# Kernel tuning notes

Measured on AMD Instinct MI355X. Metric: run time of the kernel, lower is better.

The kernel has to match this reference:

```python
import jax, jax.numpy as jnp
import numpy as np

N_NODES = 100000


def gcn_conv(x, W, b, src, dst, n_nodes):
    # x: [N, Fin], W: [Fin, Fout], edge (src->dst) with self-loops added,
    # symmetric normalization D^{-1/2} A D^{-1/2} as in PyG GCNConv defaults.
    h = x @ W  # [N, Fout]
    loops = jnp.arange(n_nodes, dtype=src.dtype)
    src_all = jnp.concatenate([src, loops])
    dst_all = jnp.concatenate([dst, loops])
    ones = jnp.ones(src_all.shape[0], dtype=h.dtype)
    deg = jax.ops.segment_sum(ones, dst_all, num_segments=n_nodes)  # in-degree incl. self-loop
    dinv = jnp.where(deg > 0, jax.lax.rsqrt(deg), 0.0)
    norm = dinv[src_all] * dinv[dst_all]  # [E+N]
    msg = h[src_all] * norm[:, None]      # gather + scale
    out = jax.ops.segment_sum(msg, dst_all, num_segments=n_nodes)  # scatter-add
    return out + b


def setup_inputs() -> dict:
    key = jax.random.key(0)
    k1, k2, k3, k4 = jax.random.split(key, 4)
    in_dim, hidden, out_dim = 128, 128, 64
    n_edges = 600000
    x = jax.random.normal(k1, (N_NODES, in_dim), dtype=jnp.float32)
    edge_index = jax.random.randint(k2, (2, n_edges), 0, N_NODES, dtype=jnp.int64)
    # Glorot-ish init for weights
    W1 = jax.random.normal(k3, (in_dim, hidden), dtype=jnp.float32) / np.sqrt(in_dim)
    b1 = jnp.zeros((hidden,), dtype=jnp.float32)
    W2 = jax.random.normal(k4, (hidden, out_dim), dtype=jnp.float32) / np.sqrt(hidden)
    b2 = jnp.zeros((out_dim,), dtype=jnp.float32)
    return {"x": x, "edge_index": edge_index, "W1": W1, "b1": b1, "W2": W2, "b2": b2}


def reference(x, edge_index, W1, b1, W2, b2):
    src, dst = edge_index[0], edge_index[1]
    h = jax.nn.relu(gcn_conv(x, W1, b1, src, dst, N_NODES))
    # dropout is identity in eval mode (training=False)
    return gcn_conv(h, W2, b2, src, dst, N_NODES)
```

## Files before the change

### kernel.cpp

```cpp
#include <hip/hip_runtime.h>
#include <hip/hip_bf16.h>
#include <stdint.h>

typedef unsigned int u32;
typedef unsigned short u16;
typedef __attribute__((ext_vector_type(8))) short short8;
typedef __attribute__((ext_vector_type(4))) float f32x4;

#define SCAN_TILE 2048

__device__ __forceinline__ float bf2f(u16 u) {
    union { u32 u; float f; } v; v.u = ((u32)u) << 16; return v.f;
}
__device__ __forceinline__ u16 f2bf(float f) {
    u32 u = __float_as_uint(f);
    u32 r = (u + 0x7FFFu + ((u >> 16) & 1u)) >> 16;
    return (u16)r;
}
__device__ __forceinline__ u32 packbf(float lo, float hi) {
    return ((u32)f2bf(hi) << 16) | (u32)f2bf(lo);
}

__global__ __launch_bounds__(256) void detect_zero_k(const u32* __restrict__ xw,
                                                     const u32* __restrict__ ew,
                                                     int* __restrict__ flags,
                                                     int* __restrict__ deg, int M) {
    const int t = threadIdx.x;
    const int i4 = (blockIdx.x * 256 + t) * 4;
    if (i4 + 4 <= M) *(int4*)(deg + i4) = make_int4(0, 0, 0, 0);
    else { for (int j = 0; j < 4; j++) if (i4 + j < M) deg[i4 + j] = 0; }

    if (blockIdx.x == 0) {
        __shared__ int cnt;
        __shared__ u32 orr;
        if (t == 0) { cnt = 0; orr = 0u; }
        __syncthreads();
        int hits = 0;
        for (int i = t; i < 1024; i += 256) {
            u32 f = (xw[i] >> 7) & 0xFFu;
            if (f >= 100u && f <= 140u) hits++;
        }
        atomicAdd(&cnt, hits);
        atomicOr(&orr, ew[2 * t + 1]);
        __syncthreads();
        if (t == 0) {
            flags[0] = (cnt < 512) ? 1 : 0;
            flags[1] = (orr == 0u) ? 1 : 0;
        }
    }
}

template<int N>
__device__ __forceinline__ void wpack_one(const void* W, uint4* wpk, int p, int f32w) {
    const int n = p & (N - 1);
    const int kb = p >> ((N == 128) ? 7 : 6);
    u32 pk[4];
    if (f32w) {
        const float* wp = (const float*)W + (size_t)(kb * 8) * N + n;
        #pragma unroll
        for (int jj = 0; jj < 4; jj++)
            pk[jj] = packbf(wp[(2 * jj) * N], wp[(2 * jj + 1) * N]);
    } else {
        const u16* wp = (const u16*)W + (size_t)(kb * 8) * N + n;
        #pragma unroll
        for (int jj = 0; jj < 4; jj++)
            pk[jj] = ((u32)wp[(2 * jj + 1) * N] << 16) | (u32)wp[(2 * jj) * N];
    }
    uint4 v; v.x = pk[0]; v.y = pk[1]; v.z = pk[2]; v.w = pk[3];
    wpk[p] = v;
}

__global__ __launch_bounds__(256) void wpack_all_k(const void* __restrict__ W1,
                                                   const void* __restrict__ W2,
                                                   uint4* __restrict__ wpk1,
                                                   uint4* __restrict__ wpk2,
                                                   const int* __restrict__ flags) {
    const int b = blockIdx.x, t = threadIdx.x;
    const int f32w = flags[0];
    if (b < 8) wpack_one<128>(W1, wpk1, b * 256 + t, f32w);
    else       wpack_one<64> (W2, wpk2, (b - 8) * 256 + t, f32w);
}

__global__ __launch_bounds__(256) void count_deg_k(const void* __restrict__ ei, int E,
                                                   const int* __restrict__ flags,
                                                   int* __restrict__ deg) {
    const int i2 = (blockIdx.x * 256 + threadIdx.x) * 2;
    if (i2 >= E) return;
    if (flags[1]) {
        const long long* dp = (const long long*)ei + E;
        if (i2 + 1 < E) {
            longlong2 v = *(const longlong2*)(dp + i2);
            atomicAdd(&deg[(int)v.x], 1);
            atomicAdd(&deg[(int)v.y], 1);
        } else atomicAdd(&deg[(int)dp[i2]], 1);
    } else {
        const int* dp = (const int*)ei + E;
        if (i2 + 1 < E) {
            int2 v = *(const int2*)(dp + i2);
            atomicAdd(&deg[v.x], 1);
            atomicAdd(&deg[v.y], 1);
        } else atomicAdd(&deg[dp[i2]], 1);
    }
}

__global__ __launch_bounds__(256) void scan_partial_k(const int* __restrict__ deg, int M,
                                                      int* __restrict__ bsum) {
    const int t = threadIdx.x;
    const int base = blockIdx.x * SCAN_TILE + t * 8;
    int s = 0;
    if (base + 8 <= M) {
        int4 a = *(const int4*)(deg + base);
        int4 b = *(const int4*)(deg + base + 4);
        s = a.x + a.y + a.z + a.w + b.x + b.y + b.z + b.w;
    } else {
        for (int j = 0; j < 8; j++) if (base + j < M) s += deg[base + j];
    }
    __shared__ int red[256];
    red[t] = s;
    __syncthreads();
    for (int d = 128; d > 0; d >>= 1) {
        if (t < d) red[t] += red[t + d];
        __syncthreads();
    }
    if (t == 0) bsum[blockIdx.x] = red[0];
}

__global__ __launch_bounds__(256) void scan_bsum_k(int* __restrict__ bsum, int nb,
                                                   int* __restrict__ off, int M) {
    __shared__ int buf[2][256];
    const int t = threadIdx.x;
    int v = (t < nb) ? bsum[t] : 0;
    const int own = v;
    buf[0][t] = v;
    __syncthreads();
    int cur = 0;
    for (int d = 1; d < 256; d <<= 1) {
        int x = buf[cur][t];
        if (t >= d) x += buf[cur][t - d];
        buf[cur ^ 1][t] = x;
        __syncthreads();
        cur ^= 1;
    }
    if (t < nb) bsum[t] = buf[cur][t] - own;
    if (t == 255) off[M] = buf[cur][255];
}

__global__ __launch_bounds__(256) void scan_final_k(const int* __restrict__ deg,
                                                    const int* __restrict__ bsum, int M,
                                                    int* __restrict__ off,
                                                    int* __restrict__ cursor,
                                                    float* __restrict__ dinv) {
    const int t = threadIdx.x;
    const int base = blockIdx.x * SCAN_TILE + t * 8;
    int v[8];
    int s = 0;
    const bool full = (base + 8 <= M);
    if (full) {
        int4 a = *(const int4*)(deg + base);
        int4 b = *(const int4*)(deg + base + 4);
        v[0] = a.x; v[1] = a.y; v[2] = a.z; v[3] = a.w;
        v[4] = b.x; v[5] = b.y; v[6] = b.z; v[7] = b.w;
        s = v[0] + v[1] + v[2] + v[3] + v[4] + v[5] + v[6] + v[7];
    } else {
        #pragma unroll
        for (int j = 0; j < 8; j++) { v[j] = (base + j < M) ? deg[base + j] : 0; s += v[j]; }
    }
    __shared__ int buf[2][256];
    buf[0][t] = s;
    __syncthreads();
    int cur = 0;
    for (int d = 1; d < 256; d <<= 1) {
        int x = buf[cur][t];
        if (t >= d) x += buf[cur][t - d];
        buf[cur ^ 1][t] = x;
        __syncthreads();
        cur ^= 1;
    }
    int pre = bsum[blockIdx.x] + buf[cur][t] - s;
    int o[8]; float dv[8];
    #pragma unroll
    for (int j = 0; j < 8; j++) {
        o[j] = pre;
        dv[j] = rsqrtf((float)(v[j] + 1));
        pre += v[j];
    }
    if (full) {
        *(int4*)(off + base)     = make_int4(o[0], o[1], o[2], o[3]);
        *(int4*)(off + base + 4) = make_int4(o[4], o[5], o[6], o[7]);
        *(int4*)(cursor + base)     = make_int4(o[0], o[1], o[2], o[3]);
        *(int4*)(cursor + base + 4) = make_int4(o[4], o[5], o[6], o[7]);
        *(float4*)(dinv + base)     = make_float4(dv[0], dv[1], dv[2], dv[3]);
        *(float4*)(dinv + base + 4) = make_float4(dv[4], dv[5], dv[6], dv[7]);
    } else {
        for (int j = 0; j < 8; j++) if (base + j < M) {
            off[base + j] = o[j]; cursor[base + j] = o[j]; dinv[base + j] = dv[j];
        }
    }
}

__global__ __launch_bounds__(256) void fill_k(const void* __restrict__ ei, int E,
                                              const int* __restrict__ flags,
                                              int* __restrict__ cursor, int* __restrict__ eidx) {
    const int i2 = (blockIdx.x * 256 + threadIdx.x) * 2;
    if (i2 >= E) return;
    int s0, d0, s1 = -1, d1 = -1;
    if (flags[1]) {
        const long long* sp = (const long long*)ei;
        const long long* dp = sp + E;
        if (i2 + 1 < E) {
            longlong2 sv = *(const longlong2*)(sp + i2);
            longlong2 dv = *(const longlong2*)(dp + i2);
            s0 = (int)sv.x; s1 = (int)sv.y; d0 = (int)dv.x; d1 = (int)dv.y;
        } else { s0 = (int)sp[i2]; d0 = (int)dp[i2]; }
    } else {
        const int* sp = (const int*)ei;
        const int* dp = sp + E;
        if (i2 + 1 < E) {
            int2 sv = *(const int2*)(sp + i2);
            int2 dv = *(const int2*)(dp + i2);
            s0 = sv.x; s1 = sv.y; d0 = dv.x; d1 = dv.y;
        } else { s0 = sp[i2]; d0 = dp[i2]; }
    }
    int p0 = atomicAdd(&cursor[d0], 1);
    eidx[p0] = s0;
    if (s1 >= 0 || d1 >= 0) {
        if (i2 + 1 < E) {
            int p1 = atomicAdd(&cursor[d1], 1);
            eidx[p1] = s1;
        }
    }
}

template<int N>
__global__ __launch_bounds__(256) void gemm_mfma_k(
    const void* __restrict__ X, const uint4* __restrict__ wpk,
    const float* __restrict__ dinv, u16* __restrict__ HS,
    const int* __restrict__ flags, int x_is_ext, int M)
{
    constexpr int NT = N / 16;
    constexpr int NC8 = N / 8;
    __shared__ u32 xlds[64 * 64];
    const int t = threadIdx.x;
    const int wave = t >> 6, lane = t & 63;
    const int q = lane >> 4, m = lane & 15;
    const bool xf32 = (x_is_ext != 0) && (flags[0] != 0);
    const int row0 = blockIdx.x * 64;

    for (int c = t; c < 1024; c += 256) {
        const int row = c >> 4, c8 = c & 15;
        const int grow = row0 + row;
        uint4 pk = make_uint4(0u, 0u, 0u, 0u);
        if (grow < M) {
            if (xf32) {
                const float* xp = (const float*)X + (size_t)grow * 128 + c8 * 8;
                float4 u = *(const float4*)xp;
                float4 v = *(const float4*)(xp + 4);
                pk.x = packbf(u.x, u.y); pk.y = packbf(u.z, u.w);
                pk.z = packbf(v.x, v.y); pk.w = packbf(v.z, v.w);
            } else {
                pk = *(const uint4*)((const u16*)X + (size_t)grow * 128 + c8 * 8);
            }
        }
        *(uint4*)&xlds[row * 64 + c8 * 4] = pk;
    }
    __syncthreads();

    union { uint4 u; short8 v; } a[4];
    #pragma unroll
    for (int s = 0; s < 4; s++)
        a[s].u = *(const uint4*)&xlds[(wave * 16 + m) * 64 + (s * 4 + q) * 4];

    f32x4 acc[NT];
    #pragma unroll
    for (int tt = 0; tt < NT; tt++)
        acc[tt] = (f32x4){0.f, 0.f, 0.f, 0.f};

    #pragma unroll
    for (int s = 0; s < 4; s++) {
        union { uint4 u; short8 v; } b[NT];
        #pragma unroll
        for (int tt = 0; tt < NT; tt++)
            b[tt].u = wpk[(s * 4 + q) * N + tt * 16 + m];
        #pragma unroll
        for (int tt = 0; tt < NT; tt++)
            acc[tt] = __builtin_amdgcn_mfma_f32_16x16x32_bf16(
                a[s].v, b[tt].v, acc[tt], 0, 0, 0);
    }

    float dv[4];
    #pragma unroll
    for (int r = 0; r < 4; r++) {
        const int grow = row0 + wave * 16 + q * 4 + r;
        dv[r] = (grow < M) ? dinv[grow] : 0.f;
    }

    u16* orow = (u16*)&xlds[wave * 16 * 64];
    #pragma unroll
    for (int tt = 0; tt < NT; tt++)
        #pragma unroll
        for (int r = 0; r < 4; r++)
            orow[(q * 4 + r) * N + tt * 16 + m] = f2bf(acc[tt][r] * dv[r]);

    constexpr int ITER = 16 * NC8 / 64;
    #pragma unroll
    for (int j = 0; j < ITER; j++) {
        const int cc = lane + j * 64;
        const int lrow = cc / NC8, c8 = cc % NC8;
        const int grow = row0 + wave * 16 + lrow;
        uint4 v = *(const uint4*)&((const u32*)orow)[lrow * (N / 2) + c8 * 4];
        if (grow < M)
            *(uint4*)(HS + (size_t)grow * N + c8 * 8) = v;
    }
}

template<int N, bool RELU>
__global__ __launch_bounds__(256) void aggregate_k(
    const u16* __restrict__ hs, const int* __restrict__ eidx,
    const int* __restrict__ off, const float* __restrict__ dinv,
    const void* __restrict__ bias, void* __restrict__ out,
    const int* __restrict__ flags, int out_is_ext, int M)
{
    constexpr int TPN = N / 8;
    constexpr int NPB = 256 / TPN;
    const int node = blockIdx.x * NPB + threadIdx.x / TPN;
    const int lane = threadIdx.x % TPN;
    if (node >= M) return;
    const int f32io = flags[0];
    const int beg = off[node], end = off[node + 1];
    const int c8 = lane * 8;
    const u16* __restrict__ hrow = hs + c8;

    float a[8];
    {
        uint4 sp = *(const uint4*)(hrow + (size_t)node * N);
        const u16* s = (const u16*)&sp;
        #pragma unroll
        for (int j = 0; j < 8; j++) a[j] = bf2f(s[j]);
    }

    int p = beg;
    for (; p + 4 <= end; p += 4) {
        const int s0 = eidx[p + 0], s1 = eidx[p + 1];
        const int s2 = eidx[p + 2], s3 = eidx[p + 3];
        uint4 v0 = *(const uint4*)(hrow + (size_t)s0 * N);
        uint4 v1 = *(const uint4*)(hrow + (size_t)s1 * N);
        uint4 v2 = *(const uint4*)(hrow + (size_t)s2 * N);
        uint4 v3 = *(const uint4*)(hrow + (size_t)s3 * N);
        const u16* q0 = (const u16*)&v0; const u16* q1 = (const u16*)&v1;
        const u16* q2 = (const u16*)&v2; const u16* q3 = (const u16*)&v3;
        #pragma unroll
        for (int j = 0; j < 8; j++)
            a[j] += (bf2f(q0[j]) + bf2f(q1[j])) + (bf2f(q2[j]) + bf2f(q3[j]));
    }
    for (; p < end; p++) {
        const int s = eidx[p];
        uint4 v = *(const uint4*)(hrow + (size_t)s * N);
        const u16* q = (const u16*)&v;
        #pragma unroll
        for (int j = 0; j < 8; j++) a[j] += bf2f(q[j]);
    }

    const float dv = dinv[node];
    float b[8];
    if (f32io) {
        float4 u = *(const float4*)((const float*)bias + c8);
        float4 v = *(const float4*)((const float*)bias + c8 + 4);
        b[0] = u.x; b[1] = u.y; b[2] = u.z; b[3] = u.w;
        b[4] = v.x; b[5] = v.y; b[6] = v.z; b[7] = v.w;
    } else {
        uint4 u = *(const uint4*)((const u16*)bias + c8);
        const u16* s = (const u16*)&u;
        #pragma unroll
        for (int j = 0; j < 8; j++) b[j] = bf2f(s[j]);
    }
    float o[8];
    #pragma unroll
    for (int j = 0; j < 8; j++) {
        o[j] = fmaf(dv, a[j], b[j]);
        if (RELU) o[j] = fmaxf(o[j], 0.f);
    }
    if (out_is_ext && f32io) {
        float* op = (float*)out + (size_t)node * N + c8;
        *(float4*)op       = make_float4(o[0], o[1], o[2], o[3]);
        *(float4*)(op + 4) = make_float4(o[4], o[5], o[6], o[7]);
    } else {
        uint4 pk;
        pk.x = packbf(o[0], o[1]); pk.y = packbf(o[2], o[3]);
        pk.z = packbf(o[4], o[5]); pk.w = packbf(o[6], o[7]);
        *(uint4*)((u16*)out + (size_t)node * N + c8) = pk;
    }
}

extern "C" void kernel_launch(void* const* d_in, const int* in_sizes, int n_in,
                              void* d_out, int out_size, void* d_ws, size_t ws_size,
                              hipStream_t stream) {
    const void* x  = d_in[0];
    const void* ei = d_in[1];
    const void* W1 = d_in[2];
    const void* b1 = d_in[3];
    const void* W2 = d_in[4];
    const void* b2 = d_in[5];

    const int M = in_sizes[0] / 128;
    const int E = in_sizes[1] / 2;
    const int NB = (M + SCAN_TILE - 1) / SCAN_TILE;

    char* ws = (char*)d_ws;
    size_t offb = 0;
    auto alloc = [&](size_t bytes) -> void* {
        void* p = ws + offb; offb += (bytes + 255) & ~(size_t)255; return p;
    };
    int*   flags  = (int*)  alloc(256);
    int*   bsum   = (int*)  alloc(1024);
    uint4* wpk1   = (uint4*)alloc(16 * 128 * 16);
    uint4* wpk2   = (uint4*)alloc(16 * 64 * 16);
    int*   deg    = (int*)  alloc((size_t)M * 4);
    int*   off    = (int*)  alloc((size_t)(M + 1) * 4);
    int*   cursor = (int*)  alloc((size_t)M * 4);
    float* dinv   = (float*)alloc((size_t)M * 4);
    int*   eidx   = (int*)  alloc((size_t)E * 4);
    u16*   hs1    = (u16*)  alloc((size_t)M * 128 * 2);
    u16*   out1   = (u16*)  alloc((size_t)M * 128 * 2);
    u16*   hs2    = (u16*)  alloc((size_t)M * 64 * 2);
    (void)ws_size; (void)n_in; (void)out_size;

    detect_zero_k<<<(M + 1023) / 1024, 256, 0, stream>>>((const u32*)x, (const u32*)ei,
                                                         flags, deg, M);
    wpack_all_k<<<12, 256, 0, stream>>>(W1, W2, wpk1, wpk2, flags);
    count_deg_k<<<(E + 511) / 512, 256, 0, stream>>>(ei, E, flags, deg);
    scan_partial_k<<<NB, 256, 0, stream>>>(deg, M, bsum);
    scan_bsum_k<<<1, 256, 0, stream>>>(bsum, NB, off, M);
    scan_final_k<<<NB, 256, 0, stream>>>(deg, bsum, M, off, cursor, dinv);
    fill_k<<<(E + 511) / 512, 256, 0, stream>>>(ei, E, flags, cursor, eidx);

    gemm_mfma_k<128><<<(M + 63) / 64, 256, 0, stream>>>(x, wpk1, dinv, hs1, flags, 1, M);
    aggregate_k<128, true><<<(M + 15) / 16, 256, 0, stream>>>(hs1, eidx, off, dinv, b1, out1,
                                                              flags, 0, M);
    gemm_mfma_k<64><<<(M + 63) / 64, 256, 0, stream>>>(out1, wpk2, dinv, hs2, flags, 0, M);
    aggregate_k<64, false><<<(M + 31) / 32, 256, 0, stream>>>(hs2, eidx, off, dinv, b2, d_out,
                                                              flags, 1, M);
}
```

Before: 243.1 us.

## Fuse prep kernels and replace three-pass scan with decoupled look-back scan

Merges the zero-init/flag-detection and weight-packing kernels into one prep kernel, where each packing block recomputes the dtype flag locally. The three-kernel degree scan (partial sums, block-sum scan, final) becomes a single-pass decoupled look-back scan that uses per-block status words in global memory. The goal is to cut kernel launches and the gaps between them in the small preprocessing stages. The look-back scan depends on blocks making forward progress and adds spin-wait latency. NB is only about 49 blocks, so the risk is small.

```diff
diff --git a/kernel.cpp b/kernel.cpp
--- a/kernel.cpp
+++ b/kernel.cpp
@@ -4,6 +4,7 @@
 
 typedef unsigned int u32;
 typedef unsigned short u16;
+typedef unsigned long long u64;
 typedef __attribute__((ext_vector_type(8))) short short8;
 typedef __attribute__((ext_vector_type(4))) float f32x4;
 
@@ -19,35 +20,6 @@
 }
 __device__ __forceinline__ u32 packbf(float lo, float hi) {
     return ((u32)f2bf(hi) << 16) | (u32)f2bf(lo);
-}
-
-__global__ __launch_bounds__(256) void detect_zero_k(const u32* __restrict__ xw,
-                                                     const u32* __restrict__ ew,
-                                                     int* __restrict__ flags,
-                                                     int* __restrict__ deg, int M) {
-    const int t = threadIdx.x;
-    const int i4 = (blockIdx.x * 256 + t) * 4;
-    if (i4 + 4 <= M) *(int4*)(deg + i4) = make_int4(0, 0, 0, 0);
-    else { for (int j = 0; j < 4; j++) if (i4 + j < M) deg[i4 + j] = 0; }
-
-    if (blockIdx.x == 0) {
-        __shared__ int cnt;
-        __shared__ u32 orr;
-        if (t == 0) { cnt = 0; orr = 0u; }
-        __syncthreads();
-        int hits = 0;
-        for (int i = t; i < 1024; i += 256) {
-            u32 f = (xw[i] >> 7) & 0xFFu;
-            if (f >= 100u && f <= 140u) hits++;
-        }
-        atomicAdd(&cnt, hits);
-        atomicOr(&orr, ew[2 * t + 1]);
-        __syncthreads();
-        if (t == 0) {
-            flags[0] = (cnt < 512) ? 1 : 0;
-            flags[1] = (orr == 0u) ? 1 : 0;
-        }
-    }
 }
 
 template<int N>
@@ -70,15 +42,46 @@
     wpk[p] = v;
 }
 
-__global__ __launch_bounds__(256) void wpack_all_k(const void* __restrict__ W1,
-                                                   const void* __restrict__ W2,
-                                                   uint4* __restrict__ wpk1,
-                                                   uint4* __restrict__ wpk2,
-                                                   const int* __restrict__ flags) {
+__global__ __launch_bounds__(256) void prep_k(const u32* __restrict__ xw,
+                                              const u32* __restrict__ ew,
+                                              int* __restrict__ flags,
+                                              int* __restrict__ deg, int M,
+                                              const void* __restrict__ W1,
+                                              const void* __restrict__ W2,
+                                              uint4* __restrict__ wpk1,
+                                              uint4* __restrict__ wpk2,
+                                              u64* __restrict__ lk, int nlk) {
     const int b = blockIdx.x, t = threadIdx.x;
-    const int f32w = flags[0];
-    if (b < 8) wpack_one<128>(W1, wpk1, b * 256 + t, f32w);
-    else       wpack_one<64> (W2, wpk2, (b - 8) * 256 + t, f32w);
+    const int i4 = (b * 256 + t) * 4;
+    if (i4 + 4 <= M) *(int4*)(deg + i4) = make_int4(0, 0, 0, 0);
+    else { for (int j = 0; j < 4; j++) if (i4 + j < M) deg[i4 + j] = 0; }
+
+    if (b < 12) {
+        __shared__ int cnt;
+        if (t == 0) cnt = 0;
+        __syncthreads();
+        int hits = 0;
+        #pragma unroll
+        for (int j = 0; j < 4; j++) {
+            u32 f = (xw[t * 4 + j] >> 7) & 0xFFu;
+            if (f >= 100u && f <= 140u) hits++;
+        }
+        atomicAdd(&cnt, hits);
+        __syncthreads();
+        const int f32w = (cnt < 512) ? 1 : 0;
+        if (b < 8) wpack_one<128>(W1, wpk1, b * 256 + t, f32w);
+        else       wpack_one<64> (W2, wpk2, (b - 8) * 256 + t, f32w);
+        if (b == 0) {
+            if (t < nlk) lk[t] = 0ull;
+            if (t == 0) flags[0] = f32w;
+            __shared__ u32 orr;
+            if (t == 0) orr = 0u;
+            __syncthreads();
+            atomicOr(&orr, ew[2 * t + 1]);
+            __syncthreads();
+            if (t == 0) flags[1] = (orr == 0u) ? 1 : 0;
+        }
+    }
 }
 
 __global__ __launch_bounds__(256) void count_deg_k(const void* __restrict__ ei, int E,
@@ -103,55 +106,13 @@
     }
 }
 
-__global__ __launch_bounds__(256) void scan_partial_k(const int* __restrict__ deg, int M,
-                                                      int* __restrict__ bsum) {
-    const int t = threadIdx.x;
-    const int base = blockIdx.x * SCAN_TILE + t * 8;
-    int s = 0;
-    if (base + 8 <= M) {
-        int4 a = *(const int4*)(deg + base);
-        int4 b = *(const int4*)(deg + base + 4);
-        s = a.x + a.y + a.z + a.w + b.x + b.y + b.z + b.w;
-    } else {
-        for (int j = 0; j < 8; j++) if (base + j < M) s += deg[base + j];
-    }
-    __shared__ int red[256];
-    red[t] = s;
-    __syncthreads();
-    for (int d = 128; d > 0; d >>= 1) {
-        if (t < d) red[t] += red[t + d];
-        __syncthreads();
-    }
-    if (t == 0) bsum[blockIdx.x] = red[0];
-}
-
-__global__ __launch_bounds__(256) void scan_bsum_k(int* __restrict__ bsum, int nb,
-                                                   int* __restrict__ off, int M) {
-    __shared__ int buf[2][256];
-    const int t = threadIdx.x;
-    int v = (t < nb) ? bsum[t] : 0;
-    const int own = v;
-    buf[0][t] = v;
-    __syncthreads();
-    int cur = 0;
-    for (int d = 1; d < 256; d <<= 1) {
-        int x = buf[cur][t];
-        if (t >= d) x += buf[cur][t - d];
-        buf[cur ^ 1][t] = x;
-        __syncthreads();
-        cur ^= 1;
-    }
-    if (t < nb) bsum[t] = buf[cur][t] - own;
-    if (t == 255) off[M] = buf[cur][255];
-}
-
-__global__ __launch_bounds__(256) void scan_final_k(const int* __restrict__ deg,
-                                                    const int* __restrict__ bsum, int M,
-                                                    int* __restrict__ off,
-                                                    int* __restrict__ cursor,
-                                                    float* __restrict__ dinv) {
-    const int t = threadIdx.x;
-    const int base = blockIdx.x * SCAN_TILE + t * 8;
+__global__ __launch_bounds__(256) void scan_lb_k(const int* __restrict__ deg, int M,
+                                                 u64* __restrict__ lk,
+                                                 int* __restrict__ off,
+                                                 int* __restrict__ cursor,
+                                                 float* __restrict__ dinv, int nb) {
+    const int bid = blockIdx.x, t = threadIdx.x;
+    const int base = bid * SCAN_TILE + t * 8;
     int v[8];
     int s = 0;
     const bool full = (base + 8 <= M);
@@ -176,7 +137,37 @@
         __syncthreads();
         cur ^= 1;
     }
-    int pre = bsum[blockIdx.x] + buf[cur][t] - s;
+    const int incl = buf[cur][t];
+    const int btotal = buf[cur][255];
+
+    __shared__ int sbase;
+    if (t == 0) {
+        if (bid == 0) {
+            __hip_atomic_store(&lk[0], (2ull << 62) | (u32)btotal,
+                               __ATOMIC_RELEASE, __HIP_MEMORY_SCOPE_AGENT);
+            sbase = 0;
+        } else {
+            __hip_atomic_store(&lk[bid], (1ull << 62) | (u32)btotal,
+                               __ATOMIC_RELEASE, __HIP_MEMORY_SCOPE_AGENT);
+            int run = 0;
+            int j = bid - 1;
+            while (j >= 0) {
+                u64 w = __hip_atomic_load(&lk[j], __ATOMIC_ACQUIRE,
+                                          __HIP_MEMORY_SCOPE_AGENT);
+                const u64 st = w >> 62;
+                if (st == 0) { __builtin_amdgcn_s_sleep(1); continue; }
+                run += (int)(w & 0xFFFFFFFFull);
+                if (st == 2ull) break;
+                j--;
+            }
+            sbase = run;
+            __hip_atomic_store(&lk[bid], (2ull << 62) | (u32)(run + btotal),
+                               __ATOMIC_RELEASE, __HIP_MEMORY_SCOPE_AGENT);
+        }
+    }
+    __syncthreads();
+
+    int pre = sbase + incl - s;
     int o[8]; float dv[8];
     #pragma unroll
     for (int j = 0; j < 8; j++) {
@@ -196,6 +187,7 @@
             off[base + j] = o[j]; cursor[base + j] = o[j]; dinv[base + j] = dv[j];
         }
     }
+    if (bid == nb - 1 && t == 255) off[M] = sbase + btotal;
 }
 
 __global__ __launch_bounds__(256) void fill_k(const void* __restrict__ ei, int E,
@@ -204,10 +196,11 @@
     const int i2 = (blockIdx.x * 256 + threadIdx.x) * 2;
     if (i2 >= E) return;
     int s0, d0, s1 = -1, d1 = -1;
+    bool two = (i2 + 1 < E);
     if (flags[1]) {
         const long long* sp = (const long long*)ei;
         const long long* dp = sp + E;
-        if (i2 + 1 < E) {
+        if (two) {
             longlong2 sv = *(const longlong2*)(sp + i2);
             longlong2 dv = *(const longlong2*)(dp + i2);
             s0 = (int)sv.x; s1 = (int)sv.y; d0 = (int)dv.x; d1 = (int)dv.y;
@@ -215,7 +208,7 @@
     } else {
         const int* sp = (const int*)ei;
         const int* dp = sp + E;
-        if (i2 + 1 < E) {
+        if (two) {
             int2 sv = *(const int2*)(sp + i2);
             int2 dv = *(const int2*)(dp + i2);
             s0 = sv.x; s1 = sv.y; d0 = dv.x; d1 = dv.y;
@@ -223,11 +216,9 @@
     }
     int p0 = atomicAdd(&cursor[d0], 1);
     eidx[p0] = s0;
-    if (s1 >= 0 || d1 >= 0) {
-        if (i2 + 1 < E) {
-            int p1 = atomicAdd(&cursor[d1], 1);
-            eidx[p1] = s1;
-        }
+    if (two) {
+        int p1 = atomicAdd(&cursor[d1], 1);
+        eidx[p1] = s1;
     }
 }
 
@@ -411,7 +402,7 @@
         void* p = ws + offb; offb += (bytes + 255) & ~(size_t)255; return p;
     };
     int*   flags  = (int*)  alloc(256);
-    int*   bsum   = (int*)  alloc(1024);
+    u64*   lk     = (u64*)  alloc(2048);
     uint4* wpk1   = (uint4*)alloc(16 * 128 * 16);
     uint4* wpk2   = (uint4*)alloc(16 * 64 * 16);
     int*   deg    = (int*)  alloc((size_t)M * 4);
@@ -424,13 +415,10 @@
     u16*   hs2    = (u16*)  alloc((size_t)M * 64 * 2);
     (void)ws_size; (void)n_in; (void)out_size;
 
-    detect_zero_k<<<(M + 1023) / 1024, 256, 0, stream>>>((const u32*)x, (const u32*)ei,
-                                                         flags, deg, M);
-    wpack_all_k<<<12, 256, 0, stream>>>(W1, W2, wpk1, wpk2, flags);
+    prep_k<<<(M + 1023) / 1024, 256, 0, stream>>>((const u32*)x, (const u32*)ei, flags,
+                                                  deg, M, W1, W2, wpk1, wpk2, lk, NB);
     count_deg_k<<<(E + 511) / 512, 256, 0, stream>>>(ei, E, flags, deg);
-    scan_partial_k<<<NB, 256, 0, stream>>>(deg, M, bsum);
-    scan_bsum_k<<<1, 256, 0, stream>>>(bsum, NB, off, M);
-    scan_final_k<<<NB, 256, 0, stream>>>(deg, bsum, M, off, cursor, dinv);
+    scan_lb_k<<<NB, 256, 0, stream>>>(deg, M, lk, off, cursor, dinv, NB);
     fill_k<<<(E + 511) / 512, 256, 0, stream>>>(ei, E, flags, cursor, eidx);
 
     gemm_mfma_k<128><<<(M + 63) / 64, 256, 0, stream>>>(x, wpk1, dinv, hs1, flags, 1, M);
```

Result: no change. 242.7 us (-0.2%).
